# Optimization experiments

Hardware: AMD Instinct MI355X
Metric: run time of the kernel (lower is better)

Reference implementation:

```python
import jax, jax.numpy as jnp
import numpy as np

C = 256
CR = 32  # C // nc_reduce

def setup_inputs() -> dict:
    key = jax.random.key(0)
    ks = jax.random.split(key, 8)
    B, H, W = 4, 64, 64
    x = jax.random.normal(ks[0], (B, C, H, W), dtype=jnp.float32)
    s_in = 1.0 / np.sqrt(C)
    Wq = jax.random.uniform(ks[1], (CR, C), jnp.float32, -s_in, s_in)
    bq = jax.random.uniform(ks[2], (CR,), jnp.float32, -s_in, s_in)
    Wk = jax.random.uniform(ks[3], (CR, C), jnp.float32, -s_in, s_in)
    bk = jax.random.uniform(ks[4], (CR,), jnp.float32, -s_in, s_in)
    Wv = jax.random.uniform(ks[5], (C, C), jnp.float32, -s_in, s_in)
    bv = jax.random.uniform(ks[6], (C,), jnp.float32, -s_in, s_in)
    gamma = jnp.zeros((1,), dtype=jnp.float32)
    return {"x": x, "Wq": Wq, "bq": bq, "Wk": Wk, "bk": bk,
            "Wv": Wv, "bv": bv, "gamma": gamma}

def reference(x, Wq, bq, Wk, bk, Wv, bv, gamma):
    B, Cc, H, W = x.shape
    N = H * W
    xf = x.reshape(B, Cc, N)                       # [B, C, N]
    # 1x1 convs == per-position channel projections
    q = jnp.einsum('dc,bcn->bdn', Wq, xf) + bq[None, :, None]  # [B, CR, N]
    k = jnp.einsum('dc,bcn->bdn', Wk, xf) + bk[None, :, None]  # [B, CR, N]
    v = jnp.einsum('dc,bcn->bdn', Wv, xf) + bv[None, :, None]  # [B, C, N]
    # energy[b,i,j] = q[:, :, i] . k[:, :, j]  (no scaling, as in source)
    energy = jnp.einsum('bdi,bdj->bij', q, k)      # [B, N, N]
    attn = jax.nn.softmax(energy, axis=-1)
    # out[b,c,i] = sum_j v[b,c,j] * attn[b,i,j]
    outv = jnp.einsum('bcj,bij->bci', v, attn)     # [B, C, N]
    out = gamma[0] * outv.reshape(B, Cc, H, W) + x
    return out
```

## Files before the change

### kernel.cpp

```cpp
#include <hip/hip_runtime.h>
#include <hip/hip_bf16.h>

#define NB 4
#define CCH 256
#define CRD 32
#define NN 4096

typedef __attribute__((ext_vector_type(8))) short short8;
typedef __attribute__((ext_vector_type(4))) float floatx4;
typedef __attribute__((ext_vector_type(4))) int intx4;
typedef __attribute__((ext_vector_type(2))) unsigned int uintx2;

__device__ __forceinline__ unsigned short f2bf(float f) {
  unsigned u = __builtin_bit_cast(unsigned, f);
  u += 0x7FFFu + ((u >> 16) & 1u);
  return (unsigned short)(u >> 16);
}

__device__ __forceinline__ unsigned short f2bf_c(float f) {
  f = fminf(fmaxf(f, -1.0e4f), 1.0e4f);
  unsigned u = __builtin_bit_cast(unsigned, f);
  u += 0x7FFFu + ((u >> 16) & 1u);
  return (unsigned short)(u >> 16);
}

__device__ __forceinline__ unsigned pack2c(float a, float b) {
  return (unsigned)f2bf_c(a) | ((unsigned)f2bf_c(b) << 16);
}

__device__ __forceinline__ float sat(float v) {
  return fminf(fmaxf(v, -1.0e30f), 1.0e30f);
}

__device__ __forceinline__ short8 ld_frag_g(const unsigned short* p) {
  return __builtin_bit_cast(short8, *(const intx4*)p);
}

__global__ __launch_bounds__(256) void gemm_qkv_fused(
    const float* __restrict__ x,
    const float* __restrict__ Wq, const float* __restrict__ bq,
    const float* __restrict__ Wk, const float* __restrict__ bk,
    const float* __restrict__ Wv, const float* __restrict__ bv,
    unsigned short* __restrict__ qT, unsigned short* __restrict__ kT,
    unsigned short* __restrict__ vv)
{
  __shared__ __align__(16) unsigned short xs[64 * 264];
  __shared__ __align__(16) unsigned short ws[64 * 264];

  const int tid  = threadIdx.x;
  const int wave = tid >> 6;
  const int lane = tid & 63;
  const int lq   = lane >> 4;
  const int lm   = lane & 15;
  const int n0   = blockIdx.x << 6;
  const int mg   = blockIdx.y;
  const int b    = blockIdx.z;

  {
    const int nn = lane;
    const int cg = wave;
    const float* xb = x + ((size_t)b << 20) + n0 + nn;
#pragma unroll
    for (int it = 0; it < 16; ++it) {
      const int c0 = it * 16 + cg * 4;
      const float v0 = xb[(size_t)(c0 + 0) << 12];
      const float v1 = xb[(size_t)(c0 + 1) << 12];
      const float v2 = xb[(size_t)(c0 + 2) << 12];
      const float v3 = xb[(size_t)(c0 + 3) << 12];
      uintx2 u;
      u[0] = pack2c(v0, v1);
      u[1] = pack2c(v2, v3);
      *(uintx2*)(xs + nn * 264 + c0) = u;
    }
  }

  const int mt_lo = mg ? 3 : 0;
  const int mt_hi = mg ? 5 : 3;

  for (int mt = mt_lo; mt < mt_hi; ++mt) {
#pragma unroll
    for (int i = 0; i < 16; ++i) {
      const int u  = i * 256 + tid;
      const int m  = u >> 6;
      const int o4 = (u & 63) * 4;
      const float* src = (mt == 0)
          ? (m < 32 ? Wq + (size_t)m * CCH : Wk + (size_t)(m - 32) * CCH)
          : Wv + (size_t)((mt - 1) * 64 + m) * CCH;
      const floatx4 f = *(const floatx4*)(src + o4);
      uintx2 uu;
      uu[0] = pack2c(f[0], f[1]);
      uu[1] = pack2c(f[2], f[3]);
      *(uintx2*)(ws + m * 264 + o4) = uu;
    }
    __syncthreads();

    floatx4 acc[4];
#pragma unroll
    for (int t = 0; t < 4; ++t) acc[t] = (floatx4){0.f, 0.f, 0.f, 0.f};

#pragma unroll
    for (int k0 = 0; k0 < 8; ++k0) {
      short8 af[4];
#pragma unroll
      for (int ms = 0; ms < 4; ++ms)
        af[ms] = __builtin_bit_cast(short8,
            *(const intx4*)(ws + (ms * 16 + lm) * 264 + k0 * 32 + lq * 8));
      const short8 bf = __builtin_bit_cast(short8,
          *(const intx4*)(xs + (wave * 16 + lm) * 264 + k0 * 32 + lq * 8));
#pragma unroll
      for (int ms = 0; ms < 4; ++ms)
        acc[ms] = __builtin_amdgcn_mfma_f32_16x16x32_bf16(af[ms], bf,
                                                          acc[ms], 0, 0, 0);
    }
    __syncthreads();

    if (mt == 0) {
      const int n = n0 + wave * 16 + lm;
#pragma unroll
      for (int ms = 0; ms < 4; ++ms) {
        const int d0 = (ms & 1) * 16 + lq * 4;
        const float* bias = (ms < 2) ? bq : bk;
        unsigned short* dst = (ms < 2) ? qT : kT;
        uintx2 u;
        u[0] = pack2c(acc[ms][0] + bias[d0],     acc[ms][1] + bias[d0 + 1]);
        u[1] = pack2c(acc[ms][2] + bias[d0 + 2], acc[ms][3] + bias[d0 + 3]);
        *(uintx2*)(dst + (size_t)(b * NN + n) * CRD + d0) = u;
      }
    } else {
      const int cb = (mt - 1) * 64;
      unsigned short* vb2 = ws;
#pragma unroll
      for (int ms = 0; ms < 4; ++ms)
#pragma unroll
        for (int r = 0; r < 4; ++r) {
          const int c = ms * 16 + lq * 4 + r;
          vb2[c * 64 + wave * 16 + lm] = f2bf_c(acc[ms][r] + bv[cb + c]);
        }
      __syncthreads();
#pragma unroll
      for (int it = 0; it < 2; ++it) {
        const int u = it * 256 + tid;
        const int m = u >> 3;
        const int o = (u & 7) * 8;
        *(intx4*)(vv + (size_t)(b * CCH + cb + m) * NN + n0 + o) =
            *(const intx4*)(vb2 + m * 64 + o);
      }
      __syncthreads();
    }
  }
}

__global__ __launch_bounds__(512) void attn_kernel(
    const float* __restrict__ x, const float* __restrict__ gamma_p,
    const unsigned short* __restrict__ qT, const unsigned short* __restrict__ kT,
    const unsigned short* __restrict__ vv, float* __restrict__ out)
{
  __shared__ __align__(16) unsigned char smem[65536 + 2 * 4 * 2176];

  const int tid  = threadIdx.x;
  const int wave = tid >> 6;
  const int wg   = wave >> 1;
  const int cs   = wave & 1;
  const int lane = tid & 63;
  const int lq   = lane >> 4;
  const int lm   = lane & 15;
  const int xcd = blockIdx.x & 7;
  const int pos = blockIdx.x >> 3;
  const int b   = xcd >> 1;
  const int i0  = (((xcd & 1) << 5) | pos) << 6;

  const unsigned short* kTb = kT + (size_t)b * NN * CRD;
  const unsigned short* vb  = vv + (size_t)b * CCH * NN;

  const short8 qf =
      ld_frag_g(qT + (size_t)(b * NN + i0 + wg * 16 + lm) * CRD + lq * 8);

  int vs_g[4];
  int vs_off[4];
#pragma unroll
  for (int m = 0; m < 4; ++m) {
    const int u  = m * 512 + tid;
    const int c  = u >> 3;
    const int jb = u & 7;
    vs_g[m]   = c * NN + jb * 8;
    vs_off[m] = c * 128 + ((jb ^ (c & 7)) * 16);
  }

  floatx4 acc[8];
#pragma unroll
  for (int t = 0; t < 8; ++t) acc[t] = (floatx4){0.f, 0.f, 0.f, 0.f};
  float lsum[4] = {0.f, 0.f, 0.f, 0.f};

  const floatx4 zf = {0.f, 0.f, 0.f, 0.f};

  intx4 vreg[4];
#pragma unroll
  for (int m = 0; m < 4; ++m)
    vreg[m] = *(const intx4*)(vb + vs_g[m]);
  short8 kf[2];
#pragma unroll
  for (int jt = 0; jt < 2; ++jt)
    kf[jt] = ld_frag_g(kTb + (size_t)((cs * 2 + jt) * 16 + lm) * CRD + lq * 8);

#pragma unroll
  for (int m = 0; m < 4; ++m)
    *(intx4*)(smem + vs_off[m]) = vreg[m];
  {
    unsigned char* pb0 = smem + 65536 + wg * 2176;
#pragma unroll
    for (int jt = 0; jt < 2; ++jt) {
      const floatx4 S = __builtin_amdgcn_mfma_f32_16x16x32_bf16(
          qf, kf[jt], zf, 0, 0, 0);
#pragma unroll
      for (int r = 0; r < 4; ++r) {
        const float p = __expf(fminf(fmaxf(S[r], -40.f), 40.f));
        lsum[r] += p;
        *(unsigned short*)(pb0 + (lq * 4 + r) * 136 +
                           (((cs * 2 + jt) * 16 + lm) << 1)) = f2bf(p);
      }
    }
  }
#pragma unroll
  for (int m = 0; m < 4; ++m)
    vreg[m] = *(const intx4*)(vb + vs_g[m] + 64);
#pragma unroll
  for (int jt = 0; jt < 2; ++jt)
    kf[jt] = ld_frag_g(kTb + (size_t)(64 + (cs * 2 + jt) * 16 + lm) * CRD +
                       lq * 8);

#pragma unroll 1
  for (int k = 0; k < 63; ++k) {
    asm volatile("s_waitcnt lgkmcnt(0)" ::: "memory");
    __builtin_amdgcn_s_barrier();

    unsigned char* vbp = smem + ((k & 1) << 15);
    unsigned char* pbp = smem + 65536 + (k & 1) * 8704 + wg * 2176;
    unsigned char* vbn = smem + (((k + 1) & 1) << 15);
    unsigned char* pbn = smem + 65536 + ((k + 1) & 1) * 8704 + wg * 2176;

#pragma unroll
    for (int m = 0; m < 4; ++m)
      *(intx4*)(vbn + vs_off[m]) = vreg[m];

#pragma unroll
    for (int jt = 0; jt < 2; ++jt) {
      const floatx4 S = __builtin_amdgcn_mfma_f32_16x16x32_bf16(
          qf, kf[jt], zf, 0, 0, 0);
#pragma unroll
      for (int r = 0; r < 4; ++r) {
        const float p = __expf(fminf(fmaxf(S[r], -40.f), 40.f));
        lsum[r] += p;
        *(unsigned short*)(pbn + (lq * 4 + r) * 136 +
                           (((cs * 2 + jt) * 16 + lm) << 1)) = f2bf(p);
      }
    }

    {
      const int j2 = ((k + 2 < 64) ? (k + 2) : 63) << 6;
#pragma unroll
      for (int m = 0; m < 4; ++m)
        vreg[m] = *(const intx4*)(vb + vs_g[m] + j2);
#pragma unroll
      for (int jt = 0; jt < 2; ++jt)
        kf[jt] = ld_frag_g(kTb +
                           (size_t)(j2 + (cs * 2 + jt) * 16 + lm) * CRD + lq * 8);
    }

#pragma unroll
    for (int ks = 0; ks < 2; ++ks) {
      const unsigned char* pa = pbp + lm * 136 + ks * 64 + lq * 16;
      struct U128 { unsigned long long a, b; } pp;
      pp.a = *(const unsigned long long*)pa;
      pp.b = *(const unsigned long long*)(pa + 8);
      const short8 pf = __builtin_bit_cast(short8, pp);
#pragma unroll
      for (int nt = 0; nt < 8; ++nt) {
        const int c = cs * 128 + nt * 16 + lm;
        const short8 vf = __builtin_bit_cast(
            short8,
            *(const intx4*)(vbp + c * 128 + (((ks * 4 + lq) ^ (lm & 7)) * 16)));
        acc[nt] = __builtin_amdgcn_mfma_f32_16x16x32_bf16(pf, vf, acc[nt],
                                                          0, 0, 0);
      }
    }
  }

  asm volatile("s_waitcnt lgkmcnt(0)" ::: "memory");
  __builtin_amdgcn_s_barrier();
  {
    const unsigned char* vbp = smem + (1 << 15);
    const unsigned char* pbp = smem + 65536 + 8704 + wg * 2176;
#pragma unroll
    for (int ks = 0; ks < 2; ++ks) {
      const unsigned char* pa = pbp + lm * 136 + ks * 64 + lq * 16;
      struct U128 { unsigned long long a, b; } pp;
      pp.a = *(const unsigned long long*)pa;
      pp.b = *(const unsigned long long*)(pa + 8);
      const short8 pf = __builtin_bit_cast(short8, pp);
#pragma unroll
      for (int nt = 0; nt < 8; ++nt) {
        const int c = cs * 128 + nt * 16 + lm;
        const short8 vf = __builtin_bit_cast(
            short8,
            *(const intx4*)(vbp + c * 128 + (((ks * 4 + lq) ^ (lm & 7)) * 16)));
        acc[nt] = __builtin_amdgcn_mfma_f32_16x16x32_bf16(pf, vf, acc[nt],
                                                          0, 0, 0);
      }
    }
  }

  __syncthreads();
  floatx4 lv;
#pragma unroll
  for (int r = 0; r < 4; ++r) lv[r] = lsum[r];
  *(floatx4*)(smem + ((wave * 64 + lane) << 4)) = lv;
  __syncthreads();
  const floatx4 lpart = *(const floatx4*)(smem + (((wave ^ 1) * 64 + lane) << 4));

  float inv[4];
#pragma unroll
  for (int r = 0; r < 4; ++r) {
    float v = lsum[r] + lpart[r];
    v += __shfl_xor(v, 1);
    v += __shfl_xor(v, 2);
    v += __shfl_xor(v, 4);
    v += __shfl_xor(v, 8);
    inv[r] = 1.0f / v;
  }

  __syncthreads();
  float* olds = (float*)smem;
  {
    const int ib = wg * 16 + lq * 4;
#pragma unroll
    for (int nt = 0; nt < 8; ++nt) {
      const int c = cs * 128 + nt * 16 + lm;
      floatx4 o;
#pragma unroll
      for (int r = 0; r < 4; ++r) o[r] = sat(acc[nt][r] * inv[r]);
      *(floatx4*)(olds + c * 68 + ib) = o;
    }
  }
  __syncthreads();

  const float gm = gamma_p[0];
#pragma unroll
  for (int pass = 0; pass < 8; ++pass) {
    const int c  = pass * 32 + (tid >> 4);
    const int i4 = (tid & 15) * 4;
    const floatx4 ov = *(const floatx4*)(olds + c * 68 + i4);
    const size_t idx = (size_t)(b * CCH + c) * NN + i0 + i4;
    const floatx4 xv = *(const floatx4*)(x + idx);
    floatx4 o;
#pragma unroll
    for (int e = 0; e < 4; ++e)
      o[e] = gm * ov[e] + xv[e];
    *(floatx4*)(out + idx) = o;
  }
}

extern "C" void kernel_launch(void* const* d_in, const int* in_sizes, int n_in,
                              void* d_out, int out_size, void* d_ws, size_t ws_size,
                              hipStream_t stream) {
  (void)in_sizes; (void)n_in; (void)out_size; (void)ws_size;
  const float* x     = (const float*)d_in[0];
  const float* Wq    = (const float*)d_in[1];
  const float* bq    = (const float*)d_in[2];
  const float* Wk    = (const float*)d_in[3];
  const float* bk    = (const float*)d_in[4];
  const float* Wv    = (const float*)d_in[5];
  const float* bv    = (const float*)d_in[6];
  const float* gamma = (const float*)d_in[7];

  unsigned short* qT = (unsigned short*)d_ws;
  unsigned short* kT = qT + (size_t)NB * NN * CRD;
  unsigned short* vv = kT + (size_t)NB * NN * CRD;

  gemm_qkv_fused<<<dim3(64, 2, 4), 256, 0, stream>>>(x, Wq, bq, Wk, bk, Wv, bv,
                                                     qT, kT, vv);
  attn_kernel<<<dim3(256, 1, 1), 512, 0, stream>>>(x, gamma, qT, kT, vv,
                                                   (float*)d_out);
}
```

Baseline: 159.1 us.

## Merge QKV projection M-groups into one 512-thread block per tile

The QKV projection kernel previously launched two blocks per (n-tile, batch), each converting the same 64-column x tile to bf16 and handling a subset of the five output tiles. It now launches one 512-thread block per (n-tile, batch) that loads x once and loops over all five output tiles, with eight waves split into four n-fragments and two m-halves. This removes the duplicated x load and conversion, at the cost of halving the grid to 256 blocks and serializing five weight-tile passes inside one block.

```diff
diff --git a/kernel.cpp b/kernel.cpp
--- a/kernel.cpp
+++ b/kernel.cpp
@@ -36,7 +36,7 @@
   return __builtin_bit_cast(short8, *(const intx4*)p);
 }
 
-__global__ __launch_bounds__(256) void gemm_qkv_fused(
+__global__ __launch_bounds__(512) void gemm_qkv_fused(
     const float* __restrict__ x,
     const float* __restrict__ Wq, const float* __restrict__ bq,
     const float* __restrict__ Wk, const float* __restrict__ bk,
@@ -49,20 +49,21 @@
 
   const int tid  = threadIdx.x;
   const int wave = tid >> 6;
+  const int nf   = wave & 3;
+  const int mh   = wave >> 2;
   const int lane = tid & 63;
   const int lq   = lane >> 4;
   const int lm   = lane & 15;
   const int n0   = blockIdx.x << 6;
-  const int mg   = blockIdx.y;
-  const int b    = blockIdx.z;
+  const int b    = blockIdx.y;
 
   {
     const int nn = lane;
     const int cg = wave;
     const float* xb = x + ((size_t)b << 20) + n0 + nn;
 #pragma unroll
-    for (int it = 0; it < 16; ++it) {
-      const int c0 = it * 16 + cg * 4;
+    for (int it = 0; it < 8; ++it) {
+      const int c0 = it * 32 + cg * 4;
       const float v0 = xb[(size_t)(c0 + 0) << 12];
       const float v1 = xb[(size_t)(c0 + 1) << 12];
       const float v2 = xb[(size_t)(c0 + 2) << 12];
@@ -74,13 +75,11 @@
     }
   }
 
-  const int mt_lo = mg ? 3 : 0;
-  const int mt_hi = mg ? 5 : 3;
-
-  for (int mt = mt_lo; mt < mt_hi; ++mt) {
-#pragma unroll
-    for (int i = 0; i < 16; ++i) {
-      const int u  = i * 256 + tid;
+#pragma unroll 1
+  for (int mt = 0; mt < 5; ++mt) {
+#pragma unroll
+    for (int i = 0; i < 8; ++i) {
+      const int u  = i * 512 + tid;
       const int m  = u >> 6;
       const int o4 = (u & 63) * 4;
       const float* src = (mt == 0)
@@ -94,33 +93,34 @@
     }
     __syncthreads();
 
-    floatx4 acc[4];
-#pragma unroll
-    for (int t = 0; t < 4; ++t) acc[t] = (floatx4){0.f, 0.f, 0.f, 0.f};
+    floatx4 acc[2];
+#pragma unroll
+    for (int t = 0; t < 2; ++t) acc[t] = (floatx4){0.f, 0.f, 0.f, 0.f};
 
 #pragma unroll
     for (int k0 = 0; k0 < 8; ++k0) {
-      short8 af[4];
-#pragma unroll
-      for (int ms = 0; ms < 4; ++ms)
+      short8 af[2];
+#pragma unroll
+      for (int ms = 0; ms < 2; ++ms)
         af[ms] = __builtin_bit_cast(short8,
-            *(const intx4*)(ws + (ms * 16 + lm) * 264 + k0 * 32 + lq * 8));
+            *(const intx4*)(ws + (mh * 32 + ms * 16 + lm) * 264 +
+                            k0 * 32 + lq * 8));
       const short8 bf = __builtin_bit_cast(short8,
-          *(const intx4*)(xs + (wave * 16 + lm) * 264 + k0 * 32 + lq * 8));
-#pragma unroll
-      for (int ms = 0; ms < 4; ++ms)
+          *(const intx4*)(xs + (nf * 16 + lm) * 264 + k0 * 32 + lq * 8));
+#pragma unroll
+      for (int ms = 0; ms < 2; ++ms)
         acc[ms] = __builtin_amdgcn_mfma_f32_16x16x32_bf16(af[ms], bf,
                                                           acc[ms], 0, 0, 0);
     }
     __syncthreads();
 
     if (mt == 0) {
-      const int n = n0 + wave * 16 + lm;
-#pragma unroll
-      for (int ms = 0; ms < 4; ++ms) {
-        const int d0 = (ms & 1) * 16 + lq * 4;
-        const float* bias = (ms < 2) ? bq : bk;
-        unsigned short* dst = (ms < 2) ? qT : kT;
+      const int n = n0 + nf * 16 + lm;
+      const float* bias = mh ? bk : bq;
+      unsigned short* dst = mh ? kT : qT;
+#pragma unroll
+      for (int ms = 0; ms < 2; ++ms) {
+        const int d0 = ms * 16 + lq * 4;
         uintx2 u;
         u[0] = pack2c(acc[ms][0] + bias[d0],     acc[ms][1] + bias[d0 + 1]);
         u[1] = pack2c(acc[ms][2] + bias[d0 + 2], acc[ms][3] + bias[d0 + 3]);
@@ -130,18 +130,16 @@
       const int cb = (mt - 1) * 64;
       unsigned short* vb2 = ws;
 #pragma unroll
-      for (int ms = 0; ms < 4; ++ms)
+      for (int ms = 0; ms < 2; ++ms)
 #pragma unroll
         for (int r = 0; r < 4; ++r) {
-          const int c = ms * 16 + lq * 4 + r;
-          vb2[c * 64 + wave * 16 + lm] = f2bf_c(acc[ms][r] + bv[cb + c]);
+          const int c = mh * 32 + ms * 16 + lq * 4 + r;
+          vb2[c * 64 + nf * 16 + lm] = f2bf_c(acc[ms][r] + bv[cb + c]);
         }
       __syncthreads();
-#pragma unroll
-      for (int it = 0; it < 2; ++it) {
-        const int u = it * 256 + tid;
-        const int m = u >> 3;
-        const int o = (u & 7) * 8;
+      {
+        const int m = tid >> 3;
+        const int o = (tid & 7) * 8;
         *(intx4*)(vv + (size_t)(b * CCH + cb + m) * NN + n0 + o) =
             *(const intx4*)(vb2 + m * 64 + o);
       }
@@ -376,8 +374,8 @@
   unsigned short* kT = qT + (size_t)NB * NN * CRD;
   unsigned short* vv = kT + (size_t)NB * NN * CRD;
 
-  gemm_qkv_fused<<<dim3(64, 2, 4), 256, 0, stream>>>(x, Wq, bq, Wk, bk, Wv, bv,
-                                                     qT, kT, vv);
+  gemm_qkv_fused<<<dim3(64, 4), 512, 0, stream>>>(x, Wq, bq, Wk, bk, Wv, bv,
+                                                  qT, kT, vv);
   attn_kernel<<<dim3(256, 1, 1), 512, 0, stream>>>(x, gamma, qT, kT, vv,
                                                    (float*)d_out);
 }
```

New measurement: 162.1 us. About the same (+1.8%).

## Double the attention key tile per iteration and swizzle the P buffer

Applied to the files above, without the earlier changes.

The main attention loop now processes 128 keys per iteration instead of 64, halving the iteration count and the number of barriers. V tiles move to a four-slot ring in shared memory, and the P tile is stored with an XOR-swizzled 256-byte row layout so each fragment is read with a single 128-bit load. This raises LDS use to 160 KB and register pressure from the larger vreg and kf buffers, which can limit occupancy or cause spills.

```diff
diff --git a/kernel.cpp b/kernel.cpp
--- a/kernel.cpp
+++ b/kernel.cpp
@@ -155,7 +155,8 @@
     const unsigned short* __restrict__ qT, const unsigned short* __restrict__ kT,
     const unsigned short* __restrict__ vv, float* __restrict__ out)
 {
-  __shared__ __align__(16) unsigned char smem[65536 + 2 * 4 * 2176];
+  __shared__ __align__(16) unsigned char smem[163840];
+  const int PB = 131072;
 
   const int tid  = threadIdx.x;
   const int wave = tid >> 6;
@@ -193,92 +194,111 @@
 
   const floatx4 zf = {0.f, 0.f, 0.f, 0.f};
 
-  intx4 vreg[4];
-#pragma unroll
-  for (int m = 0; m < 4; ++m)
-    vreg[m] = *(const intx4*)(vb + vs_g[m]);
-  short8 kf[2];
-#pragma unroll
-  for (int jt = 0; jt < 2; ++jt)
-    kf[jt] = ld_frag_g(kTb + (size_t)((cs * 2 + jt) * 16 + lm) * CRD + lq * 8);
-
-#pragma unroll
-  for (int m = 0; m < 4; ++m)
-    *(intx4*)(smem + vs_off[m]) = vreg[m];
+  intx4 vreg[2][4];
+#pragma unroll
+  for (int h = 0; h < 2; ++h)
+#pragma unroll
+    for (int m = 0; m < 4; ++m)
+      vreg[h][m] = *(const intx4*)(vb + vs_g[m] + h * 64);
+#pragma unroll
+  for (int h = 0; h < 2; ++h)
+#pragma unroll
+    for (int m = 0; m < 4; ++m)
+      *(intx4*)(smem + h * 32768 + vs_off[m]) = vreg[h][m];
+
+  short8 kf[4];
+#pragma unroll
+  for (int jt = 0; jt < 4; ++jt)
+    kf[jt] = ld_frag_g(kTb + (size_t)((cs * 4 + jt) * 16 + lm) * CRD + lq * 8);
+
   {
-    unsigned char* pb0 = smem + 65536 + wg * 2176;
-#pragma unroll
-    for (int jt = 0; jt < 2; ++jt) {
+    unsigned char* pb0 = smem + PB + wg * 4096;
+#pragma unroll
+    for (int jt = 0; jt < 4; ++jt) {
       const floatx4 S = __builtin_amdgcn_mfma_f32_16x16x32_bf16(
           qf, kf[jt], zf, 0, 0, 0);
+      const int t = cs * 4 + jt;
+      const int g = 2 * t + (lm >> 3);
 #pragma unroll
       for (int r = 0; r < 4; ++r) {
         const float p = __expf(fminf(fmaxf(S[r], -40.f), 40.f));
         lsum[r] += p;
-        *(unsigned short*)(pb0 + (lq * 4 + r) * 136 +
-                           (((cs * 2 + jt) * 16 + lm) << 1)) = f2bf(p);
-      }
-    }
-  }
-#pragma unroll
-  for (int m = 0; m < 4; ++m)
-    vreg[m] = *(const intx4*)(vb + vs_g[m] + 64);
-#pragma unroll
-  for (int jt = 0; jt < 2; ++jt)
-    kf[jt] = ld_frag_g(kTb + (size_t)(64 + (cs * 2 + jt) * 16 + lm) * CRD +
-                       lq * 8);
+        const int row = lq * 4 + r;
+        *(unsigned short*)(pb0 + row * 256 + ((g ^ row) << 4) +
+                           2 * (lm & 7)) = f2bf(p);
+      }
+    }
+  }
+#pragma unroll
+  for (int h = 0; h < 2; ++h)
+#pragma unroll
+    for (int m = 0; m < 4; ++m)
+      vreg[h][m] = *(const intx4*)(vb + vs_g[m] + 128 + h * 64);
+#pragma unroll
+  for (int jt = 0; jt < 4; ++jt)
+    kf[jt] = ld_frag_g(kTb +
+                       (size_t)(128 + (cs * 4 + jt) * 16 + lm) * CRD + lq * 8);
 
 #pragma unroll 1
-  for (int k = 0; k < 63; ++k) {
+  for (int k = 0; k < 31; ++k) {
     asm volatile("s_waitcnt lgkmcnt(0)" ::: "memory");
     __builtin_amdgcn_s_barrier();
 
-    unsigned char* vbp = smem + ((k & 1) << 15);
-    unsigned char* pbp = smem + 65536 + (k & 1) * 8704 + wg * 2176;
-    unsigned char* vbn = smem + (((k + 1) & 1) << 15);
-    unsigned char* pbn = smem + 65536 + ((k + 1) & 1) * 8704 + wg * 2176;
-
-#pragma unroll
-    for (int m = 0; m < 4; ++m)
-      *(intx4*)(vbn + vs_off[m]) = vreg[m];
-
-#pragma unroll
-    for (int jt = 0; jt < 2; ++jt) {
+    unsigned char* pbp = smem + PB + (k & 1) * 16384 + wg * 4096;
+    unsigned char* pbn = smem + PB + ((k + 1) & 1) * 16384 + wg * 4096;
+    unsigned char* vr0 = smem + (((2 * k)     & 3) << 15);
+    unsigned char* vr1 = smem + (((2 * k + 1) & 3) << 15);
+
+#pragma unroll
+    for (int h = 0; h < 2; ++h) {
+      unsigned char* vw = smem + (((2 * k + 2 + h) & 3) << 15);
+#pragma unroll
+      for (int m = 0; m < 4; ++m)
+        *(intx4*)(vw + vs_off[m]) = vreg[h][m];
+    }
+
+#pragma unroll
+    for (int jt = 0; jt < 4; ++jt) {
       const floatx4 S = __builtin_amdgcn_mfma_f32_16x16x32_bf16(
           qf, kf[jt], zf, 0, 0, 0);
+      const int t = cs * 4 + jt;
+      const int g = 2 * t + (lm >> 3);
 #pragma unroll
       for (int r = 0; r < 4; ++r) {
         const float p = __expf(fminf(fmaxf(S[r], -40.f), 40.f));
         lsum[r] += p;
-        *(unsigned short*)(pbn + (lq * 4 + r) * 136 +
-                           (((cs * 2 + jt) * 16 + lm) << 1)) = f2bf(p);
+        const int row = lq * 4 + r;
+        *(unsigned short*)(pbn + row * 256 + ((g ^ row) << 4) +
+                           2 * (lm & 7)) = f2bf(p);
       }
     }
 
     {
-      const int j2 = ((k + 2 < 64) ? (k + 2) : 63) << 6;
-#pragma unroll
-      for (int m = 0; m < 4; ++m)
-        vreg[m] = *(const intx4*)(vb + vs_g[m] + j2);
-#pragma unroll
-      for (int jt = 0; jt < 2; ++jt)
+      const int w2 = (k + 2 < 32) ? (k + 2) : 31;
+      const int j2 = w2 << 7;
+#pragma unroll
+      for (int h = 0; h < 2; ++h)
+#pragma unroll
+        for (int m = 0; m < 4; ++m)
+          vreg[h][m] = *(const intx4*)(vb + vs_g[m] + j2 + h * 64);
+#pragma unroll
+      for (int jt = 0; jt < 4; ++jt)
         kf[jt] = ld_frag_g(kTb +
-                           (size_t)(j2 + (cs * 2 + jt) * 16 + lm) * CRD + lq * 8);
-    }
-
-#pragma unroll
-    for (int ks = 0; ks < 2; ++ks) {
-      const unsigned char* pa = pbp + lm * 136 + ks * 64 + lq * 16;
-      struct U128 { unsigned long long a, b; } pp;
-      pp.a = *(const unsigned long long*)pa;
-      pp.b = *(const unsigned long long*)(pa + 8);
-      const short8 pf = __builtin_bit_cast(short8, pp);
+                           (size_t)(j2 + (cs * 4 + jt) * 16 + lm) * CRD + lq * 8);
+    }
+
+#pragma unroll
+    for (int ks = 0; ks < 4; ++ks) {
+      const unsigned char* vsb = (ks < 2) ? vr0 : vr1;
+      const int ksl = ks & 1;
+      const short8 pf = __builtin_bit_cast(short8,
+          *(const intx4*)(pbp + lm * 256 + (((ks * 4 + lq) ^ lm) << 4)));
 #pragma unroll
       for (int nt = 0; nt < 8; ++nt) {
         const int c = cs * 128 + nt * 16 + lm;
         const short8 vf = __builtin_bit_cast(
             short8,
-            *(const intx4*)(vbp + c * 128 + (((ks * 4 + lq) ^ (lm & 7)) * 16)));
+            *(const intx4*)(vsb + c * 128 + (((ksl * 4 + lq) ^ (lm & 7)) * 16)));
         acc[nt] = __builtin_amdgcn_mfma_f32_16x16x32_bf16(pf, vf, acc[nt],
                                                           0, 0, 0);
       }
@@ -288,21 +308,19 @@
   asm volatile("s_waitcnt lgkmcnt(0)" ::: "memory");
   __builtin_amdgcn_s_barrier();
   {
-    const unsigned char* vbp = smem + (1 << 15);
-    const unsigned char* pbp = smem + 65536 + 8704 + wg * 2176;
-#pragma unroll
-    for (int ks = 0; ks < 2; ++ks) {
-      const unsigned char* pa = pbp + lm * 136 + ks * 64 + lq * 16;
-      struct U128 { unsigned long long a, b; } pp;
-      pp.a = *(const unsigned long long*)pa;
-      pp.b = *(const unsigned long long*)(pa + 8);
-      const short8 pf = __builtin_bit_cast(short8, pp);
+    const unsigned char* pbp = smem + PB + 16384 + wg * 4096;
+#pragma unroll
+    for (int ks = 0; ks < 4; ++ks) {
+      const unsigned char* vsb = smem + (((ks < 2) ? 2 : 3) << 15);
+      const int ksl = ks & 1;
+      const short8 pf = __builtin_bit_cast(short8,
+          *(const intx4*)(pbp + lm * 256 + (((ks * 4 + lq) ^ lm) << 4)));
 #pragma unroll
       for (int nt = 0; nt < 8; ++nt) {
         const int c = cs * 128 + nt * 16 + lm;
         const short8 vf = __builtin_bit_cast(
             short8,
-            *(const intx4*)(vbp + c * 128 + (((ks * 4 + lq) ^ (lm & 7)) * 16)));
+            *(const intx4*)(vsb + c * 128 + (((ksl * 4 + lq) ^ (lm & 7)) * 16)));
         acc[nt] = __builtin_amdgcn_mfma_f32_16x16x32_bf16(pf, vf, acc[nt],
                                                           0, 0, 0);
       }
```

Measured after the change: 163.7 us. 2.9% more time.

## Split attention work across 16 waves per block instead of 8

Applied to the files above, without the earlier changes.

Doubles the attention block to 1024 threads: each 16-row query group is now handled by four waves, each owning 64 output channels and one 16-column key tile, instead of two waves with 128 channels and two key tiles. The per-wave accumulator, V staging and exp work are halved, giving more waves to hide latency on the 256-block grid. The row-sum reduction is rewritten to combine four partial sums through shared memory. In exchange, barrier cost grows with more waves per block, and the register budget per thread is tighter under the 1024-thread launch bound.

```diff
diff --git a/kernel.cpp b/kernel.cpp
--- a/kernel.cpp
+++ b/kernel.cpp
@@ -150,7 +150,7 @@
   }
 }
 
-__global__ __launch_bounds__(512) void attn_kernel(
+__global__ __launch_bounds__(1024) void attn_kernel(
     const float* __restrict__ x, const float* __restrict__ gamma_p,
     const unsigned short* __restrict__ qT, const unsigned short* __restrict__ kT,
     const unsigned short* __restrict__ vv, float* __restrict__ out)
@@ -159,8 +159,8 @@
 
   const int tid  = threadIdx.x;
   const int wave = tid >> 6;
-  const int wg   = wave >> 1;
-  const int cs   = wave & 1;
+  const int wg   = wave >> 2;
+  const int cs   = wave & 3;
   const int lane = tid & 63;
   const int lq   = lane >> 4;
   const int lm   = lane & 15;
@@ -175,58 +175,49 @@
   const short8 qf =
       ld_frag_g(qT + (size_t)(b * NN + i0 + wg * 16 + lm) * CRD + lq * 8);
 
-  int vs_g[4];
-  int vs_off[4];
-#pragma unroll
-  for (int m = 0; m < 4; ++m) {
-    const int u  = m * 512 + tid;
+  int vs_g[2];
+  int vs_off[2];
+#pragma unroll
+  for (int m = 0; m < 2; ++m) {
+    const int u  = m * 1024 + tid;
     const int c  = u >> 3;
     const int jb = u & 7;
     vs_g[m]   = c * NN + jb * 8;
     vs_off[m] = c * 128 + ((jb ^ (c & 7)) * 16);
   }
 
-  floatx4 acc[8];
-#pragma unroll
-  for (int t = 0; t < 8; ++t) acc[t] = (floatx4){0.f, 0.f, 0.f, 0.f};
+  floatx4 acc[4];
+#pragma unroll
+  for (int t = 0; t < 4; ++t) acc[t] = (floatx4){0.f, 0.f, 0.f, 0.f};
   float lsum[4] = {0.f, 0.f, 0.f, 0.f};
 
   const floatx4 zf = {0.f, 0.f, 0.f, 0.f};
 
-  intx4 vreg[4];
-#pragma unroll
-  for (int m = 0; m < 4; ++m)
+  intx4 vreg[2];
+#pragma unroll
+  for (int m = 0; m < 2; ++m)
     vreg[m] = *(const intx4*)(vb + vs_g[m]);
-  short8 kf[2];
-#pragma unroll
-  for (int jt = 0; jt < 2; ++jt)
-    kf[jt] = ld_frag_g(kTb + (size_t)((cs * 2 + jt) * 16 + lm) * CRD + lq * 8);
-
-#pragma unroll
-  for (int m = 0; m < 4; ++m)
+  short8 kf = ld_frag_g(kTb + (size_t)(cs * 16 + lm) * CRD + lq * 8);
+
+#pragma unroll
+  for (int m = 0; m < 2; ++m)
     *(intx4*)(smem + vs_off[m]) = vreg[m];
   {
     unsigned char* pb0 = smem + 65536 + wg * 2176;
-#pragma unroll
-    for (int jt = 0; jt < 2; ++jt) {
-      const floatx4 S = __builtin_amdgcn_mfma_f32_16x16x32_bf16(
-          qf, kf[jt], zf, 0, 0, 0);
-#pragma unroll
-      for (int r = 0; r < 4; ++r) {
-        const float p = __expf(fminf(fmaxf(S[r], -40.f), 40.f));
-        lsum[r] += p;
-        *(unsigned short*)(pb0 + (lq * 4 + r) * 136 +
-                           (((cs * 2 + jt) * 16 + lm) << 1)) = f2bf(p);
-      }
-    }
-  }
-#pragma unroll
-  for (int m = 0; m < 4; ++m)
+    const floatx4 S = __builtin_amdgcn_mfma_f32_16x16x32_bf16(
+        qf, kf, zf, 0, 0, 0);
+#pragma unroll
+    for (int r = 0; r < 4; ++r) {
+      const float p = __expf(fminf(fmaxf(S[r], -40.f), 40.f));
+      lsum[r] += p;
+      *(unsigned short*)(pb0 + (lq * 4 + r) * 136 +
+                         ((cs * 16 + lm) << 1)) = f2bf(p);
+    }
+  }
+#pragma unroll
+  for (int m = 0; m < 2; ++m)
     vreg[m] = *(const intx4*)(vb + vs_g[m] + 64);
-#pragma unroll
-  for (int jt = 0; jt < 2; ++jt)
-    kf[jt] = ld_frag_g(kTb + (size_t)(64 + (cs * 2 + jt) * 16 + lm) * CRD +
-                       lq * 8);
+  kf = ld_frag_g(kTb + (size_t)(64 + cs * 16 + lm) * CRD + lq * 8);
 
 #pragma unroll 1
   for (int k = 0; k < 63; ++k) {
@@ -239,31 +230,27 @@
     unsigned char* pbn = smem + 65536 + ((k + 1) & 1) * 8704 + wg * 2176;
 
 #pragma unroll
-    for (int m = 0; m < 4; ++m)
+    for (int m = 0; m < 2; ++m)
       *(intx4*)(vbn + vs_off[m]) = vreg[m];
 
-#pragma unroll
-    for (int jt = 0; jt < 2; ++jt) {
+    {
       const floatx4 S = __builtin_amdgcn_mfma_f32_16x16x32_bf16(
-          qf, kf[jt], zf, 0, 0, 0);
+          qf, kf, zf, 0, 0, 0);
 #pragma unroll
       for (int r = 0; r < 4; ++r) {
         const float p = __expf(fminf(fmaxf(S[r], -40.f), 40.f));
         lsum[r] += p;
         *(unsigned short*)(pbn + (lq * 4 + r) * 136 +
-                           (((cs * 2 + jt) * 16 + lm) << 1)) = f2bf(p);
+                           ((cs * 16 + lm) << 1)) = f2bf(p);
       }
     }
 
     {
       const int j2 = ((k + 2 < 64) ? (k + 2) : 63) << 6;
 #pragma unroll
-      for (int m = 0; m < 4; ++m)
+      for (int m = 0; m < 2; ++m)
         vreg[m] = *(const intx4*)(vb + vs_g[m] + j2);
-#pragma unroll
-      for (int jt = 0; jt < 2; ++jt)
-        kf[jt] = ld_frag_g(kTb +
-                           (size_t)(j2 + (cs * 2 + jt) * 16 + lm) * CRD + lq * 8);
+      kf = ld_frag_g(kTb + (size_t)(j2 + cs * 16 + lm) * CRD + lq * 8);
     }
 
 #pragma unroll
@@ -274,8 +261,8 @@
       pp.b = *(const unsigned long long*)(pa + 8);
       const short8 pf = __builtin_bit_cast(short8, pp);
 #pragma unroll
-      for (int nt = 0; nt < 8; ++nt) {
-        const int c = cs * 128 + nt * 16 + lm;
+      for (int nt = 0; nt < 4; ++nt) {
+        const int c = cs * 64 + nt * 16 + lm;
         const short8 vf = __builtin_bit_cast(
             short8,
             *(const intx4*)(vbp + c * 128 + (((ks * 4 + lq) ^ (lm & 7)) * 16)));
@@ -298,8 +285,8 @@
       pp.b = *(const unsigned long long*)(pa + 8);
       const short8 pf = __builtin_bit_cast(short8, pp);
 #pragma unroll
-      for (int nt = 0; nt < 8; ++nt) {
-        const int c = cs * 128 + nt * 16 + lm;
+      for (int nt = 0; nt < 4; ++nt) {
+        const int c = cs * 64 + nt * 16 + lm;
         const short8 vf = __builtin_bit_cast(
             short8,
             *(const intx4*)(vbp + c * 128 + (((ks * 4 + lq) ^ (lm & 7)) * 16)));
@@ -309,23 +296,34 @@
     }
   }
 
-  __syncthreads();
-  floatx4 lv;
-#pragma unroll
-  for (int r = 0; r < 4; ++r) lv[r] = lsum[r];
-  *(floatx4*)(smem + ((wave * 64 + lane) << 4)) = lv;
-  __syncthreads();
-  const floatx4 lpart = *(const floatx4*)(smem + (((wave ^ 1) * 64 + lane) << 4));
-
-  float inv[4];
 #pragma unroll
   for (int r = 0; r < 4; ++r) {
-    float v = lsum[r] + lpart[r];
+    float v = lsum[r];
     v += __shfl_xor(v, 1);
     v += __shfl_xor(v, 2);
     v += __shfl_xor(v, 4);
     v += __shfl_xor(v, 8);
-    inv[r] = 1.0f / v;
+    lsum[r] = v;
+  }
+  __syncthreads();
+  {
+    floatx4 lv;
+#pragma unroll
+    for (int r = 0; r < 4; ++r) lv[r] = lsum[r];
+    *(floatx4*)(smem + ((wave * 64 + lane) << 4)) = lv;
+  }
+  __syncthreads();
+  float inv[4];
+  {
+    floatx4 s = {0.f, 0.f, 0.f, 0.f};
+#pragma unroll
+    for (int q = 0; q < 4; ++q) {
+      const floatx4 lp =
+          *(const floatx4*)(smem + (((wg * 4 + q) * 64 + lane) << 4));
+      s = s + lp;
+    }
+#pragma unroll
+    for (int r = 0; r < 4; ++r) inv[r] = 1.0f / s[r];
   }
 
   __syncthreads();
@@ -333,8 +331,8 @@
   {
     const int ib = wg * 16 + lq * 4;
 #pragma unroll
-    for (int nt = 0; nt < 8; ++nt) {
-      const int c = cs * 128 + nt * 16 + lm;
+    for (int nt = 0; nt < 4; ++nt) {
+      const int c = cs * 64 + nt * 16 + lm;
       floatx4 o;
 #pragma unroll
       for (int r = 0; r < 4; ++r) o[r] = sat(acc[nt][r] * inv[r]);
@@ -345,8 +343,8 @@
 
   const float gm = gamma_p[0];
 #pragma unroll
-  for (int pass = 0; pass < 8; ++pass) {
-    const int c  = pass * 32 + (tid >> 4);
+  for (int pass = 0; pass < 4; ++pass) {
+    const int c  = pass * 64 + (tid >> 4);
     const int i4 = (tid & 15) * 4;
     const floatx4 ov = *(const floatx4*)(olds + c * 68 + i4);
     const size_t idx = (size_t)(b * CCH + c) * NN + i0 + i4;
@@ -378,6 +376,6 @@
 
   gemm_qkv_fused<<<dim3(64, 2, 4), 256, 0, stream>>>(x, Wq, bq, Wk, bk, Wv, bv,
                                                      qT, kT, vv);
-  attn_kernel<<<dim3(256, 1, 1), 512, 0, stream>>>(x, gamma, qT, kT, vv,
-                                                   (float*)d_out);
-}
+  attn_kernel<<<dim3(256, 1, 1), 1024, 0, stream>>>(x, gamma, qT, kT, vv,
+                                                    (float*)d_out);
+}
```

Measured after the change: 156.7 us. No clear change (-1.5%).
